# Performance work log

Hardware: AMD Instinct MI355X
Metric: run time of the kernel (lower is better)

## Reference

```python
import jax, jax.numpy as jnp
import numpy as np

N = 50000
E = 625000
D_IN = 128
D_OUT = 128
NEG_SLOPE = 0.01  # torch LeakyReLU default


def setup_inputs() -> dict:
    key = jax.random.key(0)
    k1, k2, k3, k4, k5, k6, k7, k8 = jax.random.split(key, 8)
    features = jax.random.normal(k1, (N, D_IN), dtype=jnp.float32)
    target = jax.random.randint(k2, (E,), 0, N, dtype=jnp.int64)
    neighbor = jax.random.randint(k3, (E,), 0, N, dtype=jnp.int64)
    values = jax.random.uniform(k4, (E,), dtype=jnp.float32)
    # nn.Linear params (kaiming-uniform-ish init: U(-1/sqrt(in), 1/sqrt(in)))
    bound = 1.0 / np.sqrt(D_IN)
    W1 = jax.random.uniform(k5, (D_OUT, D_IN), minval=-bound, maxval=bound, dtype=jnp.float32)
    b1 = jax.random.uniform(k6, (D_OUT,), minval=-bound, maxval=bound, dtype=jnp.float32)
    W2 = jax.random.uniform(k7, (D_OUT, D_IN), minval=-bound, maxval=bound, dtype=jnp.float32)
    b2 = jax.random.uniform(k8, (D_OUT,), minval=-bound, maxval=bound, dtype=jnp.float32)
    return {"features": features, "target": target, "neighbor": neighbor,
            "values": values, "W1": W1, "b1": b1, "W2": W2, "b2": b2}


def reference(features, target, neighbor, values, W1, b1, W2, b2):
    # gather-scale: msg[e] = features[neighbor[e]] * values[e]
    msg = features[neighbor] * values[:, None]              # (E, D_IN)
    # scatter-add into target nodes
    h_neigh = jax.ops.segment_sum(msg, target, num_segments=N)  # (N, D_IN)
    # dual linear fusion + leaky relu
    h = (features + h_neigh) @ W1.T + b1 + (features * h_neigh) @ W2.T + b2
    return jnp.where(h >= 0, h, NEG_SLOPE * h)
```

## Files before the change

### kernel.cpp

```cpp
#include <hip/hip_runtime.h>

#define D 128
#define CAP 32
#define EPT 8
#define NEG_SLOPE 0.01f

typedef float v4f __attribute__((ext_vector_type(4)));
typedef short short8 __attribute__((ext_vector_type(8)));

static __device__ __forceinline__ short f2bf(float f) {
    unsigned u = __float_as_uint(f);
    unsigned r = (u + 0x7fffu + ((u >> 16) & 1u)) >> 16;
    return (short)r;
}
static __device__ __forceinline__ float bflo(unsigned u) { return __uint_as_float(u << 16); }
static __device__ __forceinline__ float bfhi(unsigned u) { return __uint_as_float(u & 0xffff0000u); }
static __device__ __forceinline__ unsigned packbf(float x, float y) {
    return (unsigned)(unsigned short)f2bf(x) | ((unsigned)(unsigned short)f2bf(y) << 16);
}
static __device__ __forceinline__ float lrelu(float v) {
    return (v >= 0.0f) ? v : NEG_SLOPE * v;
}

__global__ __launch_bounds__(256) void convbucket_kernel(const float* __restrict__ feat,
                                                         const float* __restrict__ W1,
                                                         const float* __restrict__ W2,
                                                         const int* __restrict__ tgt,
                                                         const int* __restrict__ nbr,
                                                         const float* __restrict__ vals,
                                                         unsigned* __restrict__ featbf,
                                                         short* __restrict__ Wbf,
                                                         int* __restrict__ deg,
                                                         unsigned* __restrict__ edata,
                                                         int4* __restrict__ ovf,
                                                         int* __restrict__ ovf_cnt,
                                                         int nPairs, int E, int nbB) {
    if ((int)blockIdx.x < nbB) {
        int base = blockIdx.x * (256 * EPT) + threadIdx.x;
#pragma unroll
        for (int k = 0; k < EPT; k++) {
            int e = base + k * 256;
            if (e < E) {
                int t    = tgt[e];
                int slot = atomicAdd(&deg[t], 1);
                if (slot < CAP) {
                    unsigned ent = ((unsigned)nbr[e] << 16) |
                                   (unsigned)(unsigned short)f2bf(vals[e]);
                    edata[((unsigned)t << 5) + slot] = ent;
                } else {
                    int o = atomicAdd(ovf_cnt, 1);
                    int4 ov;
                    ov.x = t;
                    ov.y = nbr[e];
                    ov.z = __float_as_int(vals[e]);
                    ov.w = 0;
                    ovf[o] = ov;
                }
            }
        }
    } else {
        int i = (blockIdx.x - nbB) * 256 + threadIdx.x;
        if (i < nPairs) {
            float2 f = ((const float2*)feat)[i];
            featbf[i] = packbf(f.x, f.y);
        }
        if (i < D * D) {
            Wbf[i]         = f2bf(W1[i]);
            Wbf[D * D + i] = f2bf(W2[i]);
        }
    }
}

__global__ __launch_bounds__(256) void gather_kernel(const unsigned* __restrict__ featbf,
                                                     const unsigned* __restrict__ edata,
                                                     const int* __restrict__ deg,
                                                     const int4* __restrict__ ovf,
                                                     const int* __restrict__ ovf_cnt,
                                                     unsigned* __restrict__ X1,
                                                     unsigned* __restrict__ X2,
                                                     int nNodes) {
    int wid  = (blockIdx.x * 256 + threadIdx.x) >> 6;
    int lane = threadIdx.x & 63;
    if (wid >= nNodes) return;
    int d  = deg[wid];
    int dd = d < CAP ? d : CAP;

    unsigned uf = featbf[(long)wid * (D / 2) + lane];

    float ax0 = 0.f, ay0 = 0.f, ax1 = 0.f, ay1 = 0.f;
    float ax2 = 0.f, ay2 = 0.f, ax3 = 0.f, ay3 = 0.f;

    {
        const unsigned* ep = edata + ((unsigned)wid << 5);
        int dm1 = dd - 1;
        for (int j = 0; j < dd; j += 8) {
            unsigned p0 = ep[min(j + 0, dm1)];
            unsigned p1 = ep[min(j + 1, dm1)];
            unsigned p2 = ep[min(j + 2, dm1)];
            unsigned p3 = ep[min(j + 3, dm1)];
            unsigned p4 = ep[min(j + 4, dm1)];
            unsigned p5 = ep[min(j + 5, dm1)];
            unsigned p6 = ep[min(j + 6, dm1)];
            unsigned p7 = ep[min(j + 7, dm1)];
            unsigned u0 = featbf[(long)(p0 >> 16) * (D / 2) + lane];
            unsigned u1 = featbf[(long)(p1 >> 16) * (D / 2) + lane];
            unsigned u2 = featbf[(long)(p2 >> 16) * (D / 2) + lane];
            unsigned u3 = featbf[(long)(p3 >> 16) * (D / 2) + lane];
            unsigned u4 = featbf[(long)(p4 >> 16) * (D / 2) + lane];
            unsigned u5 = featbf[(long)(p5 >> 16) * (D / 2) + lane];
            unsigned u6 = featbf[(long)(p6 >> 16) * (D / 2) + lane];
            unsigned u7 = featbf[(long)(p7 >> 16) * (D / 2) + lane];
            float v0 = (j + 0 < dd) ? bflo(p0) : 0.0f;
            float v1 = (j + 1 < dd) ? bflo(p1) : 0.0f;
            float v2 = (j + 2 < dd) ? bflo(p2) : 0.0f;
            float v3 = (j + 3 < dd) ? bflo(p3) : 0.0f;
            float v4 = (j + 4 < dd) ? bflo(p4) : 0.0f;
            float v5 = (j + 5 < dd) ? bflo(p5) : 0.0f;
            float v6 = (j + 6 < dd) ? bflo(p6) : 0.0f;
            float v7 = (j + 7 < dd) ? bflo(p7) : 0.0f;
            ax0 += bflo(u0) * v0; ay0 += bfhi(u0) * v0;
            ax1 += bflo(u1) * v1; ay1 += bfhi(u1) * v1;
            ax2 += bflo(u2) * v2; ay2 += bfhi(u2) * v2;
            ax3 += bflo(u3) * v3; ay3 += bfhi(u3) * v3;
            ax0 += bflo(u4) * v4; ay0 += bfhi(u4) * v4;
            ax1 += bflo(u5) * v5; ay1 += bfhi(u5) * v5;
            ax2 += bflo(u6) * v6; ay2 += bfhi(u6) * v6;
            ax3 += bflo(u7) * v7; ay3 += bfhi(u7) * v7;
        }
    }

    if (d > CAP) {
        int cnt = *ovf_cnt;
        for (int basek = 0; basek < cnt; basek += 64) {
            int k = basek + lane;
            int t = (k < cnt) ? ovf[k].x : -1;
            unsigned long long m = __ballot(t == wid);
            while (m) {
                int b = __ffsll((long long)m) - 1;
                m &= m - 1;
                int4  ov = ovf[basek + b];
                float v  = __int_as_float(ov.z);
                unsigned u = featbf[(long)ov.y * (D / 2) + lane];
                ax0 += bflo(u) * v;
                ay0 += bfhi(u) * v;
            }
        }
    }

    float accx = (ax0 + ax1) + (ax2 + ax3);
    float accy = (ay0 + ay1) + (ay2 + ay3);
    float fx = bflo(uf), fy = bfhi(uf);
    X1[(long)wid * (D / 2) + lane] = packbf(fx + accx, fy + accy);
    X2[(long)wid * (D / 2) + lane] = packbf(fx * accx, fy * accy);
}

__global__ __launch_bounds__(512) void gemm_kernel(const short* __restrict__ X1s,
                                                   const short* __restrict__ X2s,
                                                   const short* __restrict__ Wbf,
                                                   const float* __restrict__ b1,
                                                   const float* __restrict__ b2,
                                                   float* __restrict__ out, int nNodes) {
    __shared__ __align__(16) short sW[2 * D * D];

    int tid = threadIdx.x;
    for (int c = tid; c < 4096; c += 512) {
        int r  = c >> 4;
        int cc = c & 15;
        int pp = cc ^ (r & 15);
        *(short8*)(&sW[r * D + pp * 8]) = *(const short8*)(Wbf + c * 8);
    }
    __syncthreads();

    int lane = tid & 63;
    int wid  = (blockIdx.x * 512 + tid) >> 6;
    int m0   = wid * 32;
    if (m0 >= nNodes) return;
    bool t2 = (m0 + 16) < nNodes;

    int mrow = lane & 15;
    int quad = lane >> 4;

    const short* xa1 = X1s + (long)(m0 + mrow) * D + quad * 8;
    const short* xa2 = X2s + (long)(m0 + mrow) * D + quad * 8;
    const short* xb1 = xa1 + 16 * D;
    const short* xb2 = xa2 + 16 * D;

    v4f acc[2][8];
#pragma unroll
    for (int t = 0; t < 2; t++)
#pragma unroll
        for (int i = 0; i < 8; i++) acc[t][i] = (v4f)(0.0f);

#pragma unroll
    for (int s = 0; s < 4; s++) {
        short8 a1 = *(const short8*)(xa1 + s * 32);
        short8 a2 = *(const short8*)(xa2 + s * 32);
        short8 c1, c2;
        if (t2) {
            c1 = *(const short8*)(xb1 + s * 32);
            c2 = *(const short8*)(xb2 + s * 32);
        }
        int pp = (s * 4 + quad) ^ mrow;
#pragma unroll
        for (int ot = 0; ot < 8; ot++) {
            int row = ot * 16 + mrow;
            short8 w1 = *(const short8*)(&sW[row * D + pp * 8]);
            short8 w2 = *(const short8*)(&sW[D * D + row * D + pp * 8]);
            acc[0][ot] = __builtin_amdgcn_mfma_f32_16x16x32_bf16(w1, a1, acc[0][ot], 0, 0, 0);
            acc[0][ot] = __builtin_amdgcn_mfma_f32_16x16x32_bf16(w2, a2, acc[0][ot], 0, 0, 0);
            if (t2) {
                acc[1][ot] = __builtin_amdgcn_mfma_f32_16x16x32_bf16(w1, c1, acc[1][ot], 0, 0, 0);
                acc[1][ot] = __builtin_amdgcn_mfma_f32_16x16x32_bf16(w2, c2, acc[1][ot], 0, 0, 0);
            }
        }
    }

    long n0 = (long)(m0 + mrow) * D;
    long n1 = (long)(m0 + 16 + mrow) * D;
#pragma unroll
    for (int ot = 0; ot < 8; ot++) {
        int o0 = ot * 16 + quad * 4;
        float4 bb1 = *(const float4*)(b1 + o0);
        float4 bb2 = *(const float4*)(b2 + o0);
        float4 v;
        v.x = lrelu(acc[0][ot][0] + bb1.x + bb2.x);
        v.y = lrelu(acc[0][ot][1] + bb1.y + bb2.y);
        v.z = lrelu(acc[0][ot][2] + bb1.z + bb2.z);
        v.w = lrelu(acc[0][ot][3] + bb1.w + bb2.w);
        *(float4*)(out + n0 + o0) = v;
        if (t2) {
            float4 w;
            w.x = lrelu(acc[1][ot][0] + bb1.x + bb2.x);
            w.y = lrelu(acc[1][ot][1] + bb1.y + bb2.y);
            w.z = lrelu(acc[1][ot][2] + bb1.z + bb2.z);
            w.w = lrelu(acc[1][ot][3] + bb1.w + bb2.w);
            *(float4*)(out + n1 + o0) = w;
        }
    }
}

extern "C" void kernel_launch(void* const* d_in, const int* in_sizes, int n_in,
                              void* d_out, int out_size, void* d_ws, size_t ws_size,
                              hipStream_t stream) {
    const float* feat = (const float*)d_in[0];
    const int*   tgt  = (const int*)d_in[1];
    const int*   nbr  = (const int*)d_in[2];
    const float* vals = (const float*)d_in[3];
    const float* W1   = (const float*)d_in[4];
    const float* b1   = (const float*)d_in[5];
    const float* W2   = (const float*)d_in[6];
    const float* b2   = (const float*)d_in[7];
    float*       out  = (float*)d_out;

    int E      = in_sizes[1];
    int nNodes = out_size / D;

    int*      deg     = (int*)d_ws;
    int*      ovf_cnt = deg + nNodes;
    int4*     ovf     = (int4*)(deg + nNodes + 4);
    unsigned* edata   = (unsigned*)(ovf + E);
    short*    Wbf     = (short*)(edata + (long)nNodes * CAP);
    unsigned* featbf  = (unsigned*)(Wbf + 2 * D * D);
    unsigned* X1      = featbf + (long)nNodes * (D / 2);
    unsigned* X2      = X1 + (long)nNodes * (D / 2);

    int nPairs = nNodes * (D / 2);
    int nbB    = (E + 256 * EPT - 1) / (256 * EPT);
    int nbC    = (nPairs + 255) / 256;

    hipMemsetAsync(deg, 0, (size_t)(nNodes + 4) * sizeof(int), stream);
    convbucket_kernel<<<nbB + nbC, 256, 0, stream>>>(feat, W1, W2, tgt, nbr, vals,
                                                     featbf, Wbf, deg, edata, ovf, ovf_cnt,
                                                     nPairs, E, nbB);
    gather_kernel<<<(nNodes * 64 + 255) / 256, 256, 0, stream>>>(featbf, edata, deg, ovf, ovf_cnt,
                                                                 X1, X2, nNodes);

    int nPairTiles = (nNodes + 31) / 32;
    int nBlocks    = (nPairTiles + 7) / 8;
    gemm_kernel<<<nBlocks, 512, 0, stream>>>((const short*)X1, (const short*)X2, Wbf, b1, b2, out, nNodes);
}
```

Before: 167.6 us.

## Fuse neighbor gather and dual-linear GEMM into one kernel via LDS tiles

Merges the gather kernel and the MFMA GEMM kernel into a single kernel. Each 512-thread block aggregates 128 nodes, with each wave handling 16 nodes sequentially, and writes the bf16 X1/X2 rows into swizzled shared memory. It then runs the dual GEMM from LDS. This removes the global round-trip for the X1/X2 intermediates and one launch. In exchange it uses about 128KB of LDS per block, which limits occupancy, and each wave now loops serially over 16 nodes, reducing memory-level parallelism in the latency-bound gather.

New measurement: 197.4 us. 1.18x slower.

```diff
diff --git a/kernel.cpp b/kernel.cpp
--- a/kernel.cpp
+++ b/kernel.cpp
@@ -3,6 +3,7 @@
 #define D 128
 #define CAP 32
 #define EPT 8
+#define TN 128
 #define NEG_SLOPE 0.01f
 
 typedef float v4f __attribute__((ext_vector_type(4)));
@@ -71,170 +72,145 @@
     }
 }
 
-__global__ __launch_bounds__(256) void gather_kernel(const unsigned* __restrict__ featbf,
-                                                     const unsigned* __restrict__ edata,
-                                                     const int* __restrict__ deg,
-                                                     const int4* __restrict__ ovf,
-                                                     const int* __restrict__ ovf_cnt,
-                                                     unsigned* __restrict__ X1,
-                                                     unsigned* __restrict__ X2,
-                                                     int nNodes) {
-    int wid  = (blockIdx.x * 256 + threadIdx.x) >> 6;
-    int lane = threadIdx.x & 63;
-    if (wid >= nNodes) return;
-    int d  = deg[wid];
-    int dd = d < CAP ? d : CAP;
-
-    unsigned uf = featbf[(long)wid * (D / 2) + lane];
-
-    float ax0 = 0.f, ay0 = 0.f, ax1 = 0.f, ay1 = 0.f;
-    float ax2 = 0.f, ay2 = 0.f, ax3 = 0.f, ay3 = 0.f;
-
-    {
-        const unsigned* ep = edata + ((unsigned)wid << 5);
-        int dm1 = dd - 1;
-        for (int j = 0; j < dd; j += 8) {
-            unsigned p0 = ep[min(j + 0, dm1)];
-            unsigned p1 = ep[min(j + 1, dm1)];
-            unsigned p2 = ep[min(j + 2, dm1)];
-            unsigned p3 = ep[min(j + 3, dm1)];
-            unsigned p4 = ep[min(j + 4, dm1)];
-            unsigned p5 = ep[min(j + 5, dm1)];
-            unsigned p6 = ep[min(j + 6, dm1)];
-            unsigned p7 = ep[min(j + 7, dm1)];
-            unsigned u0 = featbf[(long)(p0 >> 16) * (D / 2) + lane];
-            unsigned u1 = featbf[(long)(p1 >> 16) * (D / 2) + lane];
-            unsigned u2 = featbf[(long)(p2 >> 16) * (D / 2) + lane];
-            unsigned u3 = featbf[(long)(p3 >> 16) * (D / 2) + lane];
-            unsigned u4 = featbf[(long)(p4 >> 16) * (D / 2) + lane];
-            unsigned u5 = featbf[(long)(p5 >> 16) * (D / 2) + lane];
-            unsigned u6 = featbf[(long)(p6 >> 16) * (D / 2) + lane];
-            unsigned u7 = featbf[(long)(p7 >> 16) * (D / 2) + lane];
-            float v0 = (j + 0 < dd) ? bflo(p0) : 0.0f;
-            float v1 = (j + 1 < dd) ? bflo(p1) : 0.0f;
-            float v2 = (j + 2 < dd) ? bflo(p2) : 0.0f;
-            float v3 = (j + 3 < dd) ? bflo(p3) : 0.0f;
-            float v4 = (j + 4 < dd) ? bflo(p4) : 0.0f;
-            float v5 = (j + 5 < dd) ? bflo(p5) : 0.0f;
-            float v6 = (j + 6 < dd) ? bflo(p6) : 0.0f;
-            float v7 = (j + 7 < dd) ? bflo(p7) : 0.0f;
-            ax0 += bflo(u0) * v0; ay0 += bfhi(u0) * v0;
-            ax1 += bflo(u1) * v1; ay1 += bfhi(u1) * v1;
-            ax2 += bflo(u2) * v2; ay2 += bfhi(u2) * v2;
-            ax3 += bflo(u3) * v3; ay3 += bfhi(u3) * v3;
-            ax0 += bflo(u4) * v4; ay0 += bfhi(u4) * v4;
-            ax1 += bflo(u5) * v5; ay1 += bfhi(u5) * v5;
-            ax2 += bflo(u6) * v6; ay2 += bfhi(u6) * v6;
-            ax3 += bflo(u7) * v7; ay3 += bfhi(u7) * v7;
-        }
-    }
-
-    if (d > CAP) {
-        int cnt = *ovf_cnt;
-        for (int basek = 0; basek < cnt; basek += 64) {
-            int k = basek + lane;
-            int t = (k < cnt) ? ovf[k].x : -1;
-            unsigned long long m = __ballot(t == wid);
-            while (m) {
-                int b = __ffsll((long long)m) - 1;
-                m &= m - 1;
-                int4  ov = ovf[basek + b];
-                float v  = __int_as_float(ov.z);
-                unsigned u = featbf[(long)ov.y * (D / 2) + lane];
-                ax0 += bflo(u) * v;
-                ay0 += bfhi(u) * v;
-            }
-        }
-    }
-
-    float accx = (ax0 + ax1) + (ax2 + ax3);
-    float accy = (ay0 + ay1) + (ay2 + ay3);
-    float fx = bflo(uf), fy = bfhi(uf);
-    X1[(long)wid * (D / 2) + lane] = packbf(fx + accx, fy + accy);
-    X2[(long)wid * (D / 2) + lane] = packbf(fx * accx, fy * accy);
-}
-
-__global__ __launch_bounds__(512) void gemm_kernel(const short* __restrict__ X1s,
-                                                   const short* __restrict__ X2s,
-                                                   const short* __restrict__ Wbf,
-                                                   const float* __restrict__ b1,
-                                                   const float* __restrict__ b2,
-                                                   float* __restrict__ out, int nNodes) {
-    __shared__ __align__(16) short sW[2 * D * D];
-
-    int tid = threadIdx.x;
+__global__ __launch_bounds__(512) void fused_kernel(const unsigned* __restrict__ featbf,
+                                                    const unsigned* __restrict__ edata,
+                                                    const int* __restrict__ deg,
+                                                    const int4* __restrict__ ovf,
+                                                    const int* __restrict__ ovf_cnt,
+                                                    const short* __restrict__ Wbf,
+                                                    const float* __restrict__ b1,
+                                                    const float* __restrict__ b2,
+                                                    float* __restrict__ out, int nNodes) {
+    __shared__ __align__(16) short    sW[2 * D * D];
+    __shared__ __align__(16) unsigned sX1[TN * 64];
+    __shared__ __align__(16) unsigned sX2[TN * 64];
+
+    int tid  = threadIdx.x;
+    int wave = tid >> 6;
+    int lane = tid & 63;
+
     for (int c = tid; c < 4096; c += 512) {
         int r  = c >> 4;
         int cc = c & 15;
         int pp = cc ^ (r & 15);
         *(short8*)(&sW[r * D + pp * 8]) = *(const short8*)(Wbf + c * 8);
     }
+
+    int nodeBase = blockIdx.x * TN + wave * 16;
+    for (int t = 0; t < 16; t++) {
+        int node = nodeBase + t;
+        if (node < nNodes) {
+            int d  = deg[node];
+            int dd = d < CAP ? d : CAP;
+
+            unsigned uf = featbf[(long)node * 64 + lane];
+
+            float ax0 = 0.f, ay0 = 0.f, ax1 = 0.f, ay1 = 0.f;
+            float ax2 = 0.f, ay2 = 0.f, ax3 = 0.f, ay3 = 0.f;
+            {
+                const unsigned* ep = edata + ((unsigned)node << 5);
+                int dm1 = dd - 1;
+                for (int j = 0; j < dd; j += 8) {
+                    unsigned p0 = ep[min(j + 0, dm1)];
+                    unsigned p1 = ep[min(j + 1, dm1)];
+                    unsigned p2 = ep[min(j + 2, dm1)];
+                    unsigned p3 = ep[min(j + 3, dm1)];
+                    unsigned p4 = ep[min(j + 4, dm1)];
+                    unsigned p5 = ep[min(j + 5, dm1)];
+                    unsigned p6 = ep[min(j + 6, dm1)];
+                    unsigned p7 = ep[min(j + 7, dm1)];
+                    unsigned u0 = featbf[(long)(p0 >> 16) * 64 + lane];
+                    unsigned u1 = featbf[(long)(p1 >> 16) * 64 + lane];
+                    unsigned u2 = featbf[(long)(p2 >> 16) * 64 + lane];
+                    unsigned u3 = featbf[(long)(p3 >> 16) * 64 + lane];
+                    unsigned u4 = featbf[(long)(p4 >> 16) * 64 + lane];
+                    unsigned u5 = featbf[(long)(p5 >> 16) * 64 + lane];
+                    unsigned u6 = featbf[(long)(p6 >> 16) * 64 + lane];
+                    unsigned u7 = featbf[(long)(p7 >> 16) * 64 + lane];
+                    float v0 = (j + 0 < dd) ? bflo(p0) : 0.0f;
+                    float v1 = (j + 1 < dd) ? bflo(p1) : 0.0f;
+                    float v2 = (j + 2 < dd) ? bflo(p2) : 0.0f;
+                    float v3 = (j + 3 < dd) ? bflo(p3) : 0.0f;
+                    float v4 = (j + 4 < dd) ? bflo(p4) : 0.0f;
+                    float v5 = (j + 5 < dd) ? bflo(p5) : 0.0f;
+                    float v6 = (j + 6 < dd) ? bflo(p6) : 0.0f;
+                    float v7 = (j + 7 < dd) ? bflo(p7) : 0.0f;
+                    ax0 += bflo(u0) * v0; ay0 += bfhi(u0) * v0;
+                    ax1 += bflo(u1) * v1; ay1 += bfhi(u1) * v1;
+                    ax2 += bflo(u2) * v2; ay2 += bfhi(u2) * v2;
+                    ax3 += bflo(u3) * v3; ay3 += bfhi(u3) * v3;
+                    ax0 += bflo(u4) * v4; ay0 += bfhi(u4) * v4;
+                    ax1 += bflo(u5) * v5; ay1 += bfhi(u5) * v5;
+                    ax2 += bflo(u6) * v6; ay2 += bfhi(u6) * v6;
+                    ax3 += bflo(u7) * v7; ay3 += bfhi(u7) * v7;
+                }
+            }
+            if (d > CAP) {
+                int cnt = *ovf_cnt;
+                for (int basek = 0; basek < cnt; basek += 64) {
+                    int k = basek + lane;
+                    int tt = (k < cnt) ? ovf[k].x : -1;
+                    unsigned long long m = __ballot(tt == node);
+                    while (m) {
+                        int b = __ffsll((long long)m) - 1;
+                        m &= m - 1;
+                        int4  ov = ovf[basek + b];
+                        float v  = __int_as_float(ov.z);
+                        unsigned u = featbf[(long)ov.y * 64 + lane];
+                        ax0 += bflo(u) * v;
+                        ay0 += bfhi(u) * v;
+                    }
+                }
+            }
+            float accx = (ax0 + ax1) + (ax2 + ax3);
+            float accy = (ay0 + ay1) + (ay2 + ay3);
+            float fx = bflo(uf), fy = bfhi(uf);
+            int r_l = wave * 16 + t;
+            int pos = (((lane >> 2) ^ (r_l & 15)) << 2) | (lane & 3);
+            sX1[r_l * 64 + pos] = packbf(fx + accx, fy + accy);
+            sX2[r_l * 64 + pos] = packbf(fx * accx, fy * accy);
+        }
+    }
+
     __syncthreads();
 
-    int lane = tid & 63;
-    int wid  = (blockIdx.x * 512 + tid) >> 6;
-    int m0   = wid * 32;
-    if (m0 >= nNodes) return;
-    bool t2 = (m0 + 16) < nNodes;
-
-    int mrow = lane & 15;
-    int quad = lane >> 4;
-
-    const short* xa1 = X1s + (long)(m0 + mrow) * D + quad * 8;
-    const short* xa2 = X2s + (long)(m0 + mrow) * D + quad * 8;
-    const short* xb1 = xa1 + 16 * D;
-    const short* xb2 = xa2 + 16 * D;
-
-    v4f acc[2][8];
-#pragma unroll
-    for (int t = 0; t < 2; t++)
-#pragma unroll
-        for (int i = 0; i < 8; i++) acc[t][i] = (v4f)(0.0f);
-
-#pragma unroll
-    for (int s = 0; s < 4; s++) {
-        short8 a1 = *(const short8*)(xa1 + s * 32);
-        short8 a2 = *(const short8*)(xa2 + s * 32);
-        short8 c1, c2;
-        if (t2) {
-            c1 = *(const short8*)(xb1 + s * 32);
-            c2 = *(const short8*)(xb2 + s * 32);
-        }
-        int pp = (s * 4 + quad) ^ mrow;
+    if (nodeBase < nNodes) {
+        int mrow = lane & 15;
+        int quad = lane >> 4;
+        int m0l  = wave * 16;
+
+        v4f acc[8];
+#pragma unroll
+        for (int i = 0; i < 8; i++) acc[i] = (v4f)(0.0f);
+
+#pragma unroll
+        for (int s = 0; s < 4; s++) {
+            int cc = s * 4 + quad;
+            int px = cc ^ mrow;
+            short8 a1 = *(const short8*)(&sX1[(m0l + mrow) * 64 + px * 4]);
+            short8 a2 = *(const short8*)(&sX2[(m0l + mrow) * 64 + px * 4]);
+#pragma unroll
+            for (int ot = 0; ot < 8; ot++) {
+                int row = ot * 16 + mrow;
+                short8 w1 = *(const short8*)(&sW[row * D + px * 8]);
+                short8 w2 = *(const short8*)(&sW[D * D + row * D + px * 8]);
+                acc[ot] = __builtin_amdgcn_mfma_f32_16x16x32_bf16(w1, a1, acc[ot], 0, 0, 0);
+                acc[ot] = __builtin_amdgcn_mfma_f32_16x16x32_bf16(w2, a2, acc[ot], 0, 0, 0);
+            }
+        }
+
+        long n0 = (long)(nodeBase + mrow) * D;
 #pragma unroll
         for (int ot = 0; ot < 8; ot++) {
-            int row = ot * 16 + mrow;
-            short8 w1 = *(const short8*)(&sW[row * D + pp * 8]);
-            short8 w2 = *(const short8*)(&sW[D * D + row * D + pp * 8]);
-            acc[0][ot] = __builtin_amdgcn_mfma_f32_16x16x32_bf16(w1, a1, acc[0][ot], 0, 0, 0);
-            acc[0][ot] = __builtin_amdgcn_mfma_f32_16x16x32_bf16(w2, a2, acc[0][ot], 0, 0, 0);
-            if (t2) {
-                acc[1][ot] = __builtin_amdgcn_mfma_f32_16x16x32_bf16(w1, c1, acc[1][ot], 0, 0, 0);
-                acc[1][ot] = __builtin_amdgcn_mfma_f32_16x16x32_bf16(w2, c2, acc[1][ot], 0, 0, 0);
-            }
-        }
-    }
-
-    long n0 = (long)(m0 + mrow) * D;
-    long n1 = (long)(m0 + 16 + mrow) * D;
-#pragma unroll
-    for (int ot = 0; ot < 8; ot++) {
-        int o0 = ot * 16 + quad * 4;
-        float4 bb1 = *(const float4*)(b1 + o0);
-        float4 bb2 = *(const float4*)(b2 + o0);
-        float4 v;
-        v.x = lrelu(acc[0][ot][0] + bb1.x + bb2.x);
-        v.y = lrelu(acc[0][ot][1] + bb1.y + bb2.y);
-        v.z = lrelu(acc[0][ot][2] + bb1.z + bb2.z);
-        v.w = lrelu(acc[0][ot][3] + bb1.w + bb2.w);
-        *(float4*)(out + n0 + o0) = v;
-        if (t2) {
-            float4 w;
-            w.x = lrelu(acc[1][ot][0] + bb1.x + bb2.x);
-            w.y = lrelu(acc[1][ot][1] + bb1.y + bb2.y);
-            w.z = lrelu(acc[1][ot][2] + bb1.z + bb2.z);
-            w.w = lrelu(acc[1][ot][3] + bb1.w + bb2.w);
-            *(float4*)(out + n1 + o0) = w;
+            int o0 = ot * 16 + quad * 4;
+            float4 bb1 = *(const float4*)(b1 + o0);
+            float4 bb2 = *(const float4*)(b2 + o0);
+            float4 v;
+            v.x = lrelu(acc[ot][0] + bb1.x + bb2.x);
+            v.y = lrelu(acc[ot][1] + bb1.y + bb2.y);
+            v.z = lrelu(acc[ot][2] + bb1.z + bb2.z);
+            v.w = lrelu(acc[ot][3] + bb1.w + bb2.w);
+            *(float4*)(out + n0 + o0) = v;
         }
     }
 }
@@ -261,8 +237,6 @@
     unsigned* edata   = (unsigned*)(ovf + E);
     short*    Wbf     = (short*)(edata + (long)nNodes * CAP);
     unsigned* featbf  = (unsigned*)(Wbf + 2 * D * D);
-    unsigned* X1      = featbf + (long)nNodes * (D / 2);
-    unsigned* X2      = X1 + (long)nNodes * (D / 2);
 
     int nPairs = nNodes * (D / 2);
     int nbB    = (E + 256 * EPT - 1) / (256 * EPT);
@@ -272,10 +246,8 @@
     convbucket_kernel<<<nbB + nbC, 256, 0, stream>>>(feat, W1, W2, tgt, nbr, vals,
                                                      featbf, Wbf, deg, edata, ovf, ovf_cnt,
                                                      nPairs, E, nbB);
-    gather_kernel<<<(nNodes * 64 + 255) / 256, 256, 0, stream>>>(featbf, edata, deg, ovf, ovf_cnt,
-                                                                 X1, X2, nNodes);
-
-    int nPairTiles = (nNodes + 31) / 32;
-    int nBlocks    = (nPairTiles + 7) / 8;
-    gemm_kernel<<<nBlocks, 512, 0, stream>>>((const short*)X1, (const short*)X2, Wbf, b1, b2, out, nNodes);
-}
+
+    int nBlocks = (nNodes + TN - 1) / TN;
+    fused_kernel<<<nBlocks, 512, 0, stream>>>(featbf, edata, deg, ovf, ovf_cnt,
+                                              Wbf, b1, b2, out, nNodes);
+}
```
